# Kernel optimization log

Hardware: AMD Instinct MI355X
Metric: run time of the kernel (lower is better)

Reference implementation:

```python
import jax, jax.numpy as jnp
import numpy as np

N_NODES = 8192
N_UND = 65536      # undirected pairs placed
N_DIR = 131072     # extra directed edges placed


def _build_graph():
    rng = np.random.default_rng(0)
    A = np.zeros((N_NODES, N_NODES), np.float32)
    # undirected pairs (i<j), both directions set
    ii = rng.integers(0, N_NODES, 4 * N_UND)
    jj = rng.integers(0, N_NODES, 4 * N_UND)
    m = ii < jj
    iu, ju = ii[m][:N_UND], jj[m][:N_UND]
    A[iu, ju] = 1.0
    A[ju, iu] = 1.0
    # extra directed edges
    di = rng.integers(0, N_NODES, 2 * N_DIR)
    dj = rng.integers(0, N_NODES, 2 * N_DIR)
    m2 = di != dj
    A[di[m2][:N_DIR], dj[m2][:N_DIR]] = 1.0
    # dense_to_sparse: row, col of nonzeros
    row, col = np.nonzero(A)
    edge_index = np.stack([row, col]).astype(np.int32)
    # undirected mask: A==1 & A.T==1, upper triangle
    und = np.triu((A == 1.0) & (A.T == 1.0))
    u, v = np.nonzero(und)
    undirected_edges = np.stack([u, v], axis=1).astype(np.int32)
    return A, edge_index, undirected_edges


def setup_inputs() -> dict:
    key = jax.random.key(0)
    ks = jax.random.split(key, 4)
    A, edge_index, undirected_edges = _build_graph()
    N = N_NODES
    return {
        "adjacency": jnp.asarray(A),
        "W1": jax.random.normal(ks[0], (N, 16), jnp.float32) * 0.05,
        "b1": jnp.zeros((16,), jnp.float32),
        "W2": jax.random.normal(ks[1], (16, 8), jnp.float32) * 0.25,
        "b2": jnp.zeros((8,), jnp.float32),
        "Wfc": jax.random.normal(ks[2], (16, 1), jnp.float32) * 0.25,
        "bfc": jnp.zeros((1,), jnp.float32),
        "edge_index": jnp.asarray(edge_index),
        "undirected_edges": jnp.asarray(undirected_edges),
    }


def reference(adjacency, W1, b1, W2, b2, Wfc, bfc, edge_index, undirected_edges):
    N = adjacency.shape[0]
    src, dst = edge_index[0], edge_index[1]
    E = src.shape[0]
    # GCN normalization with self-loops (PyG gcn_norm): deg over target nodes
    deg = jax.ops.segment_sum(jnp.ones((E,), adjacency.dtype), dst,
                              num_segments=N) + 1.0
    dinv = jax.lax.rsqrt(deg)                       # deg >= 1, no inf
    norm = dinv[src] * dinv[dst]                    # [E]
    self_w = (dinv * dinv)[:, None]                 # self-loop coeff [N,1]

    def conv(h):  # h: [N, F] -> normalized scatter-add aggregation
        msg = norm[:, None] * h[src]                # [E, F]
        return jax.ops.segment_sum(msg, dst, num_segments=N) + self_w * h

    # node_features = eye(N), so eye(N) @ W1 == W1
    x = jax.nn.relu(conv(W1) + b1)                  # [N, 16]
    x = jax.nn.relu(conv(x @ W2) + b2)              # [N, 8]

    u, v = undirected_edges[:, 0], undirected_edges[:, 1]
    ef = jnp.concatenate([x[u], x[v]], axis=1)      # [U, 16]
    orient = jax.nn.sigmoid(ef @ Wfc + bfc)[:, 0]   # [U]

    out = adjacency.at[u, v].set(orient).at[v, u].set(1.0 - orient)
    return out
```

## Files before the change

### kernel.cpp

```cpp
#include <hip/hip_runtime.h>
#include <math.h>

#define F1 16
#define F2 8

typedef float f32x4 __attribute__((ext_vector_type(4)));

__global__ void k_prep(const int* __restrict__ src, const int* __restrict__ dst,
                       int* __restrict__ degi, float* __restrict__ val,
                       int* __restrict__ rowptr, int E, int N) {
    int id = blockIdx.x * blockDim.x + threadIdx.x;
    if (id < E) {
        atomicAdd(&degi[dst[id]], 1);
        val[id] = 1.0f;
    }
    if (id <= N) {
        int lo = 0, hi = E;
        while (lo < hi) {
            int mid = (lo + hi) >> 1;
            if (src[mid] < id) lo = mid + 1; else hi = mid;
        }
        rowptr[id] = lo;
    }
}

__global__ void k_conv1_edges(const int* __restrict__ src, const int* __restrict__ dst,
                              const int* __restrict__ degi, const float* __restrict__ W1,
                              float* __restrict__ x1, int E) {
    int id = blockIdx.x * blockDim.x + threadIdx.x;
    int e = id >> 4;
    int f = id & (F1 - 1);
    if (e < E) {
        int s = src[e], d = dst[e];
        float nrm = rsqrtf((float)((degi[s] + 1) * (degi[d] + 1)));
        atomicAdd(&x1[(long)d * F1 + f], nrm * W1[(long)s * F1 + f]);
    }
}

__global__ void k_layer1(const int* __restrict__ degi, const float* __restrict__ b1,
                         const float* __restrict__ W1, const float* __restrict__ W2,
                         const float* __restrict__ x1, float* __restrict__ h2, int N) {
    int id = blockIdx.x * blockDim.x + threadIdx.x;
    if (id < N * F2) {
        int i = id >> 3;
        int g = id & (F2 - 1);
        float sw = 1.0f / (float)(degi[i] + 1);
        float acc = 0.0f;
        #pragma unroll
        for (int f = 0; f < F1; ++f) {
            float v = x1[(long)i * F1 + f] + sw * W1[(long)i * F1 + f] + b1[f];
            v = v > 0.0f ? v : 0.0f;
            acc += v * W2[f * F2 + g];
        }
        h2[(long)i * F2 + g] = acc;
    }
}

__global__ void k_conv2_edges(const int* __restrict__ src, const int* __restrict__ dst,
                              const int* __restrict__ degi, const float* __restrict__ h2,
                              float* __restrict__ x2, int E) {
    int id = blockIdx.x * blockDim.x + threadIdx.x;
    int e = id >> 3;
    int g = id & (F2 - 1);
    if (e < E) {
        int s = src[e], d = dst[e];
        float nrm = rsqrtf((float)((degi[s] + 1) * (degi[d] + 1)));
        atomicAdd(&x2[(long)d * F2 + g], nrm * h2[(long)s * F2 + g]);
    }
}

__global__ void k_orient2(const int2* __restrict__ ue, const float* __restrict__ x2,
                          const float* __restrict__ h2, const int* __restrict__ degi,
                          const float* __restrict__ b2, const float* __restrict__ Wfc,
                          const float* __restrict__ bfc, const int* __restrict__ rowptr,
                          const int* __restrict__ dst, float* __restrict__ val, int U) {
    int k = blockIdx.x * blockDim.x + threadIdx.x;
    if (k >= U) return;
    int2 e = ue[k];
    int u = e.x, v = e.y;
    float swu = 1.0f / (float)(degi[u] + 1);
    float swv = 1.0f / (float)(degi[v] + 1);
    float s = bfc[0];
    #pragma unroll
    for (int g = 0; g < F2; ++g) {
        float xu = x2[(long)u * F2 + g] + swu * h2[(long)u * F2 + g] + b2[g];
        float xv = x2[(long)v * F2 + g] + swv * h2[(long)v * F2 + g] + b2[g];
        xu = xu > 0.0f ? xu : 0.0f;
        xv = xv > 0.0f ? xv : 0.0f;
        s += xu * Wfc[g] + xv * Wfc[F2 + g];
    }
    float o = 1.0f / (1.0f + expf(-s));
    int lo = rowptr[u], hi = rowptr[u + 1];
    while (lo < hi) { int mid = (lo + hi) >> 1; if (dst[mid] < v) lo = mid + 1; else hi = mid; }
    if (lo < rowptr[u + 1] && dst[lo] == v) val[lo] = o;
    lo = rowptr[v]; hi = rowptr[v + 1];
    while (lo < hi) { int mid = (lo + hi) >> 1; if (dst[mid] < u) lo = mid + 1; else hi = mid; }
    if (lo < rowptr[v + 1] && dst[lo] == u) val[lo] = 1.0f - o;
}

__global__ void __launch_bounds__(256) k_writeout(const int* __restrict__ rowptr,
                                                  const int* __restrict__ dst,
                                                  const float* __restrict__ val,
                                                  float* __restrict__ out, int N) {
    int row = blockIdx.x;
    int t = threadIdx.x;
    int n4 = N >> 2;
    f32x4* out4 = (f32x4*)(out + (long)row * N);
    f32x4 z = {0.0f, 0.0f, 0.0f, 0.0f};
    for (int j = t; j < n4; j += 256) out4[j] = z;
    __syncthreads();
    int r0 = rowptr[row], r1 = rowptr[row + 1];
    float* orow = out + (long)row * N;
    for (int k = r0 + t; k < r1; k += 256) orow[dst[k]] = val[k];
}

extern "C" void kernel_launch(void* const* d_in, const int* in_sizes, int n_in,
                              void* d_out, int out_size, void* d_ws, size_t ws_size,
                              hipStream_t stream) {
    const float* W1  = (const float*)d_in[1];
    const float* b1  = (const float*)d_in[2];
    const float* W2  = (const float*)d_in[3];
    const float* b2  = (const float*)d_in[4];
    const float* Wfc = (const float*)d_in[5];
    const float* bfc = (const float*)d_in[6];
    const int* edge_index = (const int*)d_in[7];
    const int2* und       = (const int2*)d_in[8];

    int N = in_sizes[1] / F1;
    int E = in_sizes[7] / 2;
    int U = in_sizes[8] / 2;
    const int* src = edge_index;
    const int* dst = edge_index + E;

    int*   degi   = (int*)d_ws;
    float* x1     = (float*)(degi + N);
    float* x2     = x1 + (long)F1 * N;
    float* h2     = x2 + (long)F2 * N;
    int*   rowptr = (int*)(h2 + (long)F2 * N);
    float* val    = (float*)(rowptr + N + 1);

    const int B = 256;

    (void)hipMemsetAsync(d_ws, 0, (size_t)(N + (long)F1 * N + (long)F2 * N) * sizeof(float), stream);

    {
        int work = (E > N + 1) ? E : (N + 1);
        k_prep<<<(work + B - 1) / B, B, 0, stream>>>(src, dst, degi, val, rowptr, E, N);
    }
    {
        long work = (long)E * F1;
        k_conv1_edges<<<(int)((work + B - 1) / B), B, 0, stream>>>(src, dst, degi, W1, x1, E);
    }
    k_layer1<<<(N * F2 + B - 1) / B, B, 0, stream>>>(degi, b1, W1, W2, x1, h2, N);
    {
        long work = (long)E * F2;
        k_conv2_edges<<<(int)((work + B - 1) / B), B, 0, stream>>>(src, dst, degi, h2, x2, E);
    }
    k_orient2<<<(U + B - 1) / B, B, 0, stream>>>(und, x2, h2, degi, b2, Wfc, bfc,
                                                 rowptr, dst, val, U);
    k_writeout<<<N, B, 0, stream>>>(rowptr, dst, val, (float*)d_out, N);
}
```

Before: 452.5 us.

## Factor GCN norm into per-node scaling and replicate atomic accumulators

Splits the symmetric normalization into a per-node dinv so each edge message no longer needs two degree lookups and an rsqrt. Source features are pre-scaled by dinv and the destination scaling is applied after aggregation. Atomic accumulation targets are spread across 4 replica buffers chosen by edge index, to reduce same-address contention, and the replicas are summed in the consumer kernels. This costs an extra kernel, a larger memset and extra reads of the replicas.

```diff
diff --git a/kernel.cpp b/kernel.cpp
--- a/kernel.cpp
+++ b/kernel.cpp
@@ -3,6 +3,8 @@
 
 #define F1 16
 #define F2 8
+#define C1 4
+#define C2 4
 
 typedef float f32x4 __attribute__((ext_vector_type(4)));
 
@@ -24,67 +26,89 @@
     }
 }
 
+__global__ void k_wn1(const int* __restrict__ degi, const float* __restrict__ W1,
+                      float* __restrict__ dinv, float* __restrict__ Wn1, int N) {
+    int id = blockIdx.x * blockDim.x + threadIdx.x;
+    if (id < N * F1) {
+        int i = id >> 4;
+        float di = rsqrtf((float)(degi[i] + 1));
+        if ((id & (F1 - 1)) == 0) dinv[i] = di;
+        Wn1[id] = di * W1[id];
+    }
+}
+
 __global__ void k_conv1_edges(const int* __restrict__ src, const int* __restrict__ dst,
-                              const int* __restrict__ degi, const float* __restrict__ W1,
-                              float* __restrict__ x1, int E) {
+                              const float* __restrict__ Wn1, float* __restrict__ x1,
+                              int E, int N) {
     int id = blockIdx.x * blockDim.x + threadIdx.x;
     int e = id >> 4;
     int f = id & (F1 - 1);
     if (e < E) {
         int s = src[e], d = dst[e];
-        float nrm = rsqrtf((float)((degi[s] + 1) * (degi[d] + 1)));
-        atomicAdd(&x1[(long)d * F1 + f], nrm * W1[(long)s * F1 + f]);
+        float* rep = x1 + (long)(e & (C1 - 1)) * F1 * N;
+        atomicAdd(&rep[(long)d * F1 + f], Wn1[(long)s * F1 + f]);
     }
 }
 
-__global__ void k_layer1(const int* __restrict__ degi, const float* __restrict__ b1,
-                         const float* __restrict__ W1, const float* __restrict__ W2,
-                         const float* __restrict__ x1, float* __restrict__ h2, int N) {
+__global__ void k_layer1(const float* __restrict__ dinv, const float* __restrict__ b1,
+                         const float* __restrict__ Wn1, const float* __restrict__ W2,
+                         const float* __restrict__ x1, float* __restrict__ h2n, int N) {
     int id = blockIdx.x * blockDim.x + threadIdx.x;
     if (id < N * F2) {
         int i = id >> 3;
         int g = id & (F2 - 1);
-        float sw = 1.0f / (float)(degi[i] + 1);
+        float di = dinv[i];
         float acc = 0.0f;
         #pragma unroll
         for (int f = 0; f < F1; ++f) {
-            float v = x1[(long)i * F1 + f] + sw * W1[(long)i * F1 + f] + b1[f];
+            long off = (long)i * F1 + f;
+            float sum = Wn1[off];
+            #pragma unroll
+            for (int c = 0; c < C1; ++c) sum += x1[(long)c * F1 * N + off];
+            float v = di * sum + b1[f];
             v = v > 0.0f ? v : 0.0f;
             acc += v * W2[f * F2 + g];
         }
-        h2[(long)i * F2 + g] = acc;
+        h2n[(long)i * F2 + g] = di * acc;
     }
 }
 
 __global__ void k_conv2_edges(const int* __restrict__ src, const int* __restrict__ dst,
-                              const int* __restrict__ degi, const float* __restrict__ h2,
-                              float* __restrict__ x2, int E) {
+                              const float* __restrict__ h2n, float* __restrict__ x2,
+                              int E, int N) {
     int id = blockIdx.x * blockDim.x + threadIdx.x;
     int e = id >> 3;
     int g = id & (F2 - 1);
     if (e < E) {
         int s = src[e], d = dst[e];
-        float nrm = rsqrtf((float)((degi[s] + 1) * (degi[d] + 1)));
-        atomicAdd(&x2[(long)d * F2 + g], nrm * h2[(long)s * F2 + g]);
+        float* rep = x2 + (long)(e & (C2 - 1)) * F2 * N;
+        atomicAdd(&rep[(long)d * F2 + g], h2n[(long)s * F2 + g]);
     }
 }
 
 __global__ void k_orient2(const int2* __restrict__ ue, const float* __restrict__ x2,
-                          const float* __restrict__ h2, const int* __restrict__ degi,
+                          const float* __restrict__ h2n, const float* __restrict__ dinv,
                           const float* __restrict__ b2, const float* __restrict__ Wfc,
                           const float* __restrict__ bfc, const int* __restrict__ rowptr,
-                          const int* __restrict__ dst, float* __restrict__ val, int U) {
+                          const int* __restrict__ dst, float* __restrict__ val,
+                          int U, int N) {
     int k = blockIdx.x * blockDim.x + threadIdx.x;
     if (k >= U) return;
     int2 e = ue[k];
     int u = e.x, v = e.y;
-    float swu = 1.0f / (float)(degi[u] + 1);
-    float swv = 1.0f / (float)(degi[v] + 1);
+    float du = dinv[u], dv = dinv[v];
     float s = bfc[0];
     #pragma unroll
     for (int g = 0; g < F2; ++g) {
-        float xu = x2[(long)u * F2 + g] + swu * h2[(long)u * F2 + g] + b2[g];
-        float xv = x2[(long)v * F2 + g] + swv * h2[(long)v * F2 + g] + b2[g];
+        float su = h2n[(long)u * F2 + g];
+        float sv = h2n[(long)v * F2 + g];
+        #pragma unroll
+        for (int c = 0; c < C2; ++c) {
+            su += x2[(long)c * F2 * N + (long)u * F2 + g];
+            sv += x2[(long)c * F2 * N + (long)v * F2 + g];
+        }
+        float xu = du * su + b2[g];
+        float xv = dv * sv + b2[g];
         xu = xu > 0.0f ? xu : 0.0f;
         xv = xv > 0.0f ? xv : 0.0f;
         s += xu * Wfc[g] + xv * Wfc[F2 + g];
@@ -134,29 +158,32 @@
 
     int*   degi   = (int*)d_ws;
     float* x1     = (float*)(degi + N);
-    float* x2     = x1 + (long)F1 * N;
-    float* h2     = x2 + (long)F2 * N;
-    int*   rowptr = (int*)(h2 + (long)F2 * N);
+    float* x2     = x1 + (long)C1 * F1 * N;
+    float* dinv   = x2 + (long)C2 * F2 * N;
+    float* Wn1    = dinv + N;
+    float* h2n    = Wn1 + (long)F1 * N;
+    int*   rowptr = (int*)(h2n + (long)F2 * N);
     float* val    = (float*)(rowptr + N + 1);
 
     const int B = 256;
-
-    (void)hipMemsetAsync(d_ws, 0, (size_t)(N + (long)F1 * N + (long)F2 * N) * sizeof(float), stream);
+    long nz = (long)N * (1 + C1 * F1 + C2 * F2);
+    (void)hipMemsetAsync(d_ws, 0, (size_t)nz * sizeof(float), stream);
 
     {
         int work = (E > N + 1) ? E : (N + 1);
         k_prep<<<(work + B - 1) / B, B, 0, stream>>>(src, dst, degi, val, rowptr, E, N);
     }
+    k_wn1<<<(N * F1 + B - 1) / B, B, 0, stream>>>(degi, W1, dinv, Wn1, N);
     {
         long work = (long)E * F1;
-        k_conv1_edges<<<(int)((work + B - 1) / B), B, 0, stream>>>(src, dst, degi, W1, x1, E);
+        k_conv1_edges<<<(int)((work + B - 1) / B), B, 0, stream>>>(src, dst, Wn1, x1, E, N);
     }
-    k_layer1<<<(N * F2 + B - 1) / B, B, 0, stream>>>(degi, b1, W1, W2, x1, h2, N);
+    k_layer1<<<(N * F2 + B - 1) / B, B, 0, stream>>>(dinv, b1, Wn1, W2, x1, h2n, N);
     {
         long work = (long)E * F2;
-        k_conv2_edges<<<(int)((work + B - 1) / B), B, 0, stream>>>(src, dst, degi, h2, x2, E);
+        k_conv2_edges<<<(int)((work + B - 1) / B), B, 0, stream>>>(src, dst, h2n, x2, E, N);
     }
-    k_orient2<<<(U + B - 1) / B, B, 0, stream>>>(und, x2, h2, degi, b2, Wfc, bfc,
-                                                 rowptr, dst, val, U);
+    k_orient2<<<(U + B - 1) / B, B, 0, stream>>>(und, x2, h2n, dinv, b2, Wfc, bfc,
+                                                 rowptr, dst, val, U, N);
     k_writeout<<<N, B, 0, stream>>>(rowptr, dst, val, (float*)d_out, N);
 }
```

After: 457.8 us. About the same (+1.2%).
